# Optimization experiments

Hardware: AMD Instinct MI355X
Metric: run time of the kernel (lower is better)

Reference implementation:

```python
import jax, jax.numpy as jnp
import numpy as np

B, H, N, D = 2, 16, 2048, 64


def setup_inputs() -> dict:
    key = jax.random.key(0)
    kq, kk, kv = jax.random.split(key, 3)
    q = jax.random.normal(kq, (B, H, N, D), dtype=jnp.float32)
    k = jax.random.normal(kk, (B, H, N, D), dtype=jnp.float32)
    v = jax.random.normal(kv, (B, H, N, D), dtype=jnp.float32)
    return {"q": q, "k": k, "v": v}


def reference(q, k, v):
    b, h, n, d = q.shape
    # add_zero_kv: prepend an all-zero key/value along the sequence dim
    k = jnp.pad(k, ((0, 0), (0, 0), (1, 0), (0, 0)))  # [b,h,n+1,d]
    v = jnp.pad(v, ((0, 0), (0, 0), (1, 0), (0, 0)))
    kv_len = n + 1

    # l2_distance augmentation: q'.k' = 2 q.k - |q|^2 - |k|^2 = -|q - k|^2
    k_sq = jnp.sum(k * k, axis=-1, keepdims=True)
    k_aug = jnp.concatenate([k, -jnp.ones_like(k_sq), k_sq], axis=-1)  # [b,h,kv,d+2]
    q_sq = jnp.sum(q * q, axis=-1, keepdims=True)
    q_aug = jnp.concatenate([2.0 * q, q_sq, -jnp.ones_like(q_sq)], axis=-1)  # [b,h,n,d+2]

    # SDPA default scale uses the AUGMENTED head dim (d + 2)
    scale = (d + 2) ** -0.5
    scores = jnp.einsum('bhid,bhjd->bhij', q_aug, k_aug) * scale  # [b,h,n,kv]

    # causal mask folded into boolean mask because kv_len > q_len:
    # create_causal_mask(n, kv) = triu(ones, kv - n + 1) masked; allowed where j <= i + (kv - n)
    i = jnp.arange(n)[:, None]
    j = jnp.arange(kv_len)[None, :]
    allowed = j <= i + (kv_len - n)  # [n, kv]

    neg = jnp.asarray(-jnp.inf, dtype=scores.dtype)
    scores = jnp.where(allowed[None, None], scores, neg)
    attn = jax.nn.softmax(scores, axis=-1)
    out = jnp.einsum('bhij,bhjd->bhid', attn, v)  # [b,h,n,d]
    return out
```

## Files before the change

### kernel.cpp

```cpp
#include <hip/hip_runtime.h>


#define NQ 2048
#define DH 64
#define NT 32

typedef float f32x4 __attribute__((ext_vector_type(4)));
typedef __bf16 bf16x8 __attribute__((ext_vector_type(8)));
typedef unsigned short u16x8 __attribute__((ext_vector_type(8)));

union B8 { u16x8 u; bf16x8 b; };

__device__ __forceinline__ unsigned short f2b(float f) {
  unsigned int x = __builtin_bit_cast(unsigned int, f);
  unsigned int r = x + 0x7fffu + ((x >> 16) & 1u);
  return (unsigned short)(r >> 16);
}
__device__ __forceinline__ float b2f(unsigned short u) {
  unsigned int t = ((unsigned int)u) << 16;
  return __builtin_bit_cast(float, t);
}

__device__ __forceinline__ int kslot(int a) {
  return (a & 0x23) | ((a & 0x04) << 2) | ((a & 0x18) >> 1);
}

__device__ __forceinline__ void gl_lds16(const void* g, void* l) {
  __builtin_amdgcn_global_load_lds(
      (const __attribute__((address_space(1))) unsigned int*)g,
      (__attribute__((address_space(3))) unsigned int*)l, 16, 0, 0);
}
__device__ __forceinline__ void gl_lds4(const void* g, void* l) {
  __builtin_amdgcn_global_load_lds(
      (const __attribute__((address_space(1))) unsigned int*)g,
      (__attribute__((address_space(3))) unsigned int*)l, 4, 0, 0);
}

constexpr float QS = 0.3551784733906239f;
constexpr float BS = 0.17758923669531197f;

__global__ __launch_bounds__(256) void build_ws(
    const float* __restrict__ k, const float* __restrict__ v,
    unsigned short* __restrict__ wsK, unsigned short* __restrict__ wsV,
    float* __restrict__ wsB)
{
  const int bh = blockIdx.x;
  const int t  = blockIdx.y;
  const int tid  = threadIdx.x;
  const int wid  = tid >> 6;
  const int lane = tid & 63;
  const size_t bhN = (size_t)bh * NQ;
  const int tile64 = t * 64;
  const size_t tileId = (size_t)bh * NT + t;
  unsigned short* Kt = wsK + tileId * 4096;
  unsigned short* Vt = wsV + tileId * 4096;
  float*          Bt = wsB + tileId * 64;

  __shared__ float sTb[64];

#pragma unroll
  for (int i = 0; i < 4; i++) {
    int f  = i * 256 + tid;
    int kg = f >> 4, d4 = f & 15;
    int slot = kslot(kg);
    const float4* kp = (const float4*)(k + (bhN + tile64 + kg) * DH);
    float4 kk = kp[d4];
    unsigned short h0 = f2b(kk.x), h1 = f2b(kk.y), h2 = f2b(kk.z), h3 = f2b(kk.w);
    float a0 = b2f(h0), a1 = b2f(h1), a2 = b2f(h2), a3 = b2f(h3);
    float ss = a0*a0 + a1*a1 + a2*a2 + a3*a3;
    ss += __shfl_xor(ss, 1, 64);
    ss += __shfl_xor(ss, 2, 64);
    ss += __shfl_xor(ss, 4, 64);
    ss += __shfl_xor(ss, 8, 64);
    if (d4 == 0) {
      float tb = __builtin_amdgcn_exp2f(-BS * ss);
      Bt[slot] = tb;
      sTb[kg]  = tb;
    }
    unsigned int w0 = (unsigned int)h0 | ((unsigned int)h1 << 16);
    unsigned int w1 = (unsigned int)h2 | ((unsigned int)h3 << 16);
    int idx = slot * 64 + ((d4 * 4) ^ ((slot & 7) << 3));
    uint2 wv; wv.x = w0; wv.y = w1;
    *(uint2*)&Kt[idx] = wv;
  }
  __syncthreads();

#pragma unroll
  for (int jj = 0; jj < 4; jj++) {
    int kgb = jj * 16 + wid * 4;
    const float* vp = v + (bhN + tile64 + kgb) * DH + lane;
    float x0 = vp[0] * sTb[kgb + 0];
    float x1 = vp[DH] * sTb[kgb + 1];
    float x2 = vp[2 * DH] * sTb[kgb + 2];
    float x3 = vp[3 * DH] * sTb[kgb + 3];
    unsigned int w0 = (unsigned int)f2b(x0) | ((unsigned int)f2b(x1) << 16);
    unsigned int w1 = (unsigned int)f2b(x2) | ((unsigned int)f2b(x3) << 16);
    int idx = lane * 64 + (kgb ^ ((lane & 7) << 3));
    uint2 wv; wv.x = w0; wv.y = w1;
    *(uint2*)&Vt[idx] = wv;
  }
}

__global__ __launch_bounds__(256) void attend_l2_flash(
    const float* __restrict__ q,
    const unsigned short* __restrict__ wsK,
    const unsigned short* __restrict__ wsV,
    const float* __restrict__ wsB,
    float* __restrict__ out)
{
  const int bh   = blockIdx.x;
  const int qt   = (gridDim.y - 1) - blockIdx.y;
  const int qbase = qt * 64;
  const int tid  = threadIdx.x;
  const int wid  = tid >> 6;
  const int lane = tid & 63;
  const int g    = lane >> 4;
  const int qi   = lane & 15;
  const int qg   = qbase + wid * 16 + qi;
  const size_t bhN = (size_t)bh * NQ;

  __shared__ __align__(16) unsigned short sK[2][4096];
  __shared__ __align__(16) unsigned short sV[2][4096];
  __shared__ __align__(16) float sB[2][64];

  const float* qrow = q + (bhN + qg) * DH;
  bf16x8 q8[2];
#pragma unroll
  for (int ks = 0; ks < 2; ks++) {
    B8 th;
#pragma unroll
    for (int j = 0; j < 8; j++)
      th.u[j] = f2b(qrow[ks * 32 + g * 8 + j] * QS);
    q8[ks] = th.b;
  }

  f32x4 oacc[4] = { {0,0,0,0}, {0,0,0,0}, {0,0,0,0}, {0,0,0,0} };
  f32x4 l4 = {0, 0, 0, 0};

  const int ntiles = qt + 1;
  const size_t tbase = (size_t)bh * NT;

  auto STAGE = [&](int buf, int t) {
    const char* Kt = (const char*)(wsK + (tbase + t) * 4096);
    const char* Vt = (const char*)(wsV + (tbase + t) * 4096);
#pragma unroll
    for (int c = 0; c < 2; c++) {
      int boff = wid * 2048 + c * 1024;
      gl_lds16(Kt + boff + lane * 16, (char*)&sK[buf][0] + boff);
      gl_lds16(Vt + boff + lane * 16, (char*)&sV[buf][0] + boff);
    }
    if (wid == 0) {
      const char* Bt = (const char*)(wsB + (tbase + t) * 64);
      gl_lds4(Bt + lane * 4, (char*)&sB[buf][0]);
    }
  };

  int cur = 0;
  STAGE(0, 0);
  __syncthreads();

  for (int t = 0; t < ntiles; t++) {
    if (t + 1 < ntiles) STAGE(cur ^ 1, t + 1);

    f32x4 sc[4] = { {0,0,0,0}, {0,0,0,0}, {0,0,0,0}, {0,0,0,0} };
#pragma unroll
    for (int c = 0; c < 4; c++) {
#pragma unroll
      for (int ks = 0; ks < 2; ks++) {
        int idx = (16 * c + qi) * 64 + ((ks * 32 + g * 8) ^ ((qi & 7) << 3));
        bf16x8 ak = *(const bf16x8*)&sK[cur][idx];
        sc[c] = __builtin_amdgcn_mfma_f32_16x16x32_bf16(ak, q8[ks], sc[c], 0, 0, 0);
      }
    }

    const bool diag = (t == ntiles - 1);
    if (diag) {
      const int tile64 = t * 64;
#pragma unroll
      for (int c = 0; c < 4; c++)
#pragma unroll
        for (int r = 0; r < 4; r++) {
          int key = tile64 + 32 * (c >> 1) + 8 * g + 4 * (c & 1) + r;
          if (key > qg) sc[c][r] = -1e30f;
        }
    }

#pragma unroll
    for (int c = 0; c < 4; c++) {
      f32x4 tb = *(const f32x4*)&sB[cur][16 * c + 4 * g];
#pragma unroll
      for (int r = 0; r < 4; r++) sc[c][r] = __builtin_amdgcn_exp2f(sc[c][r]);
#pragma unroll
      for (int r = 0; r < 4; r++) l4[r] = __builtin_fmaf(sc[c][r], tb[r], l4[r]);
    }

    B8 t0, t1;
#pragma unroll
    for (int j = 0; j < 8; j++) {
      t0.b[j] = (__bf16)sc[(j >> 2)][j & 3];
      t1.b[j] = (__bf16)sc[2 + (j >> 2)][j & 3];
    }

#pragma unroll
    for (int db = 0; db < 4; db++) {
#pragma unroll
      for (int ks = 0; ks < 2; ks++) {
        int idx = (db * 16 + qi) * 64 + ((ks * 32 + g * 8) ^ ((qi & 7) << 3));
        bf16x8 av = *(const bf16x8*)&sV[cur][idx];
        oacc[db] = __builtin_amdgcn_mfma_f32_16x16x32_bf16(av, (ks ? t1.b : t0.b),
                                                           oacc[db], 0, 0, 0);
      }
    }
    __syncthreads();
    cur ^= 1;
  }

  float lt = (l4[0] + l4[1]) + (l4[2] + l4[3]);
  lt += __shfl_xor(lt, 16, 64);
  lt += __shfl_xor(lt, 32, 64);
  float denom = lt + 1.0f;
  float inv = 1.0f / denom;
  float* op = out + (bhN + qg) * DH;
#pragma unroll
  for (int db = 0; db < 4; db++) {
    float4 o;
    o.x = oacc[db][0] * inv;
    o.y = oacc[db][1] * inv;
    o.z = oacc[db][2] * inv;
    o.w = oacc[db][3] * inv;
    *(float4*)(op + db * 16 + 4 * g) = o;
  }
}

extern "C" void kernel_launch(void* const* d_in, const int* in_sizes, int n_in,
                              void* d_out, int out_size, void* d_ws, size_t ws_size,
                              hipStream_t stream) {
  (void)in_sizes; (void)n_in; (void)out_size; (void)ws_size;
  const float* q = (const float*)d_in[0];
  const float* k = (const float*)d_in[1];
  const float* v = (const float*)d_in[2];
  float* out = (float*)d_out;

  char* ws = (char*)d_ws;
  unsigned short* wsK = (unsigned short*)ws;
  unsigned short* wsV = (unsigned short*)(ws + (8u << 20));
  float*          wsB = (float*)(ws + (16u << 20));

  build_ws<<<dim3(32, NT), dim3(256), 0, stream>>>(k, v, wsK, wsV, wsB);
  attend_l2_flash<<<dim3(32, NT), dim3(256), 0, stream>>>(q, wsK, wsV, wsB, out);
}
```

Baseline: 52.61 us.

## Triple-buffer K/V tiles with manual vmcnt waits and register-load bias terms

New measurement: 49.15 us, median of 2. 1.07x faster.

```diff
diff --git a/kernel.cpp b/kernel.cpp
--- a/kernel.cpp
+++ b/kernel.cpp
@@ -29,11 +29,6 @@
   __builtin_amdgcn_global_load_lds(
       (const __attribute__((address_space(1))) unsigned int*)g,
       (__attribute__((address_space(3))) unsigned int*)l, 16, 0, 0);
-}
-__device__ __forceinline__ void gl_lds4(const void* g, void* l) {
-  __builtin_amdgcn_global_load_lds(
-      (const __attribute__((address_space(1))) unsigned int*)g,
-      (__attribute__((address_space(3))) unsigned int*)l, 4, 0, 0);
 }
 
 constexpr float QS = 0.3551784733906239f;
@@ -119,9 +114,8 @@
   const int qg   = qbase + wid * 16 + qi;
   const size_t bhN = (size_t)bh * NQ;
 
-  __shared__ __align__(16) unsigned short sK[2][4096];
-  __shared__ __align__(16) unsigned short sV[2][4096];
-  __shared__ __align__(16) float sB[2][64];
+  __shared__ __align__(16) unsigned short sK[3][4096];
+  __shared__ __align__(16) unsigned short sV[3][4096];
 
   const float* qrow = q + (bhN + qg) * DH;
   bf16x8 q8[2];
@@ -139,28 +133,45 @@
 
   const int ntiles = qt + 1;
   const size_t tbase = (size_t)bh * NT;
-
-  auto STAGE = [&](int buf, int t) {
+  const float* TB = wsB + tbase * 64;
+
+  auto LTB = [&](int t, f32x4* tb) {
+    const float* p = TB + t * 64 + 4 * g;
+#pragma unroll
+    for (int c = 0; c < 4; c++) tb[c] = *(const f32x4*)(p + 16 * c);
+  };
+  auto STAGE = [&](unsigned short* bK, unsigned short* bV, int t) {
     const char* Kt = (const char*)(wsK + (tbase + t) * 4096);
     const char* Vt = (const char*)(wsV + (tbase + t) * 4096);
 #pragma unroll
     for (int c = 0; c < 2; c++) {
       int boff = wid * 2048 + c * 1024;
-      gl_lds16(Kt + boff + lane * 16, (char*)&sK[buf][0] + boff);
-      gl_lds16(Vt + boff + lane * 16, (char*)&sV[buf][0] + boff);
-    }
-    if (wid == 0) {
-      const char* Bt = (const char*)(wsB + (tbase + t) * 64);
-      gl_lds4(Bt + lane * 4, (char*)&sB[buf][0]);
+      gl_lds16(Kt + boff + lane * 16, (char*)bK + boff);
+      gl_lds16(Vt + boff + lane * 16, (char*)bV + boff);
     }
   };
 
-  int cur = 0;
-  STAGE(0, 0);
-  __syncthreads();
+  unsigned short *kA = sK[0], *kB = sK[1], *kC = sK[2];
+  unsigned short *vA = sV[0], *vB = sV[1], *vC = sV[2];
+  f32x4 tb_cur[4], tb_nxt[4];
+
+  STAGE(kA, vA, 0);
+  LTB(0, tb_cur);
+  if (ntiles > 1) {
+    STAGE(kB, vB, 1);
+    asm volatile("s_waitcnt vmcnt(4)" ::: "memory");
+  } else {
+    asm volatile("s_waitcnt vmcnt(0)" ::: "memory");
+  }
+  __builtin_amdgcn_s_barrier();
 
   for (int t = 0; t < ntiles; t++) {
-    if (t + 1 < ntiles) STAGE(cur ^ 1, t + 1);
+    const bool hasN1 = (t + 1 < ntiles);
+    const bool hasN2 = (t + 2 < ntiles);
+    if (hasN1) LTB(t + 1, tb_nxt);
+    __builtin_amdgcn_sched_barrier(0);
+    if (hasN2) STAGE(kC, vC, t + 2);
+    __builtin_amdgcn_sched_barrier(0);
 
     f32x4 sc[4] = { {0,0,0,0}, {0,0,0,0}, {0,0,0,0}, {0,0,0,0} };
 #pragma unroll
@@ -168,13 +179,12 @@
 #pragma unroll
       for (int ks = 0; ks < 2; ks++) {
         int idx = (16 * c + qi) * 64 + ((ks * 32 + g * 8) ^ ((qi & 7) << 3));
-        bf16x8 ak = *(const bf16x8*)&sK[cur][idx];
+        bf16x8 ak = *(const bf16x8*)&kA[idx];
         sc[c] = __builtin_amdgcn_mfma_f32_16x16x32_bf16(ak, q8[ks], sc[c], 0, 0, 0);
       }
     }
 
-    const bool diag = (t == ntiles - 1);
-    if (diag) {
+    if (t == ntiles - 1) {
       const int tile64 = t * 64;
 #pragma unroll
       for (int c = 0; c < 4; c++)
@@ -187,11 +197,10 @@
 
 #pragma unroll
     for (int c = 0; c < 4; c++) {
-      f32x4 tb = *(const f32x4*)&sB[cur][16 * c + 4 * g];
 #pragma unroll
       for (int r = 0; r < 4; r++) sc[c][r] = __builtin_amdgcn_exp2f(sc[c][r]);
 #pragma unroll
-      for (int r = 0; r < 4; r++) l4[r] = __builtin_fmaf(sc[c][r], tb[r], l4[r]);
+      for (int r = 0; r < 4; r++) l4[r] = __builtin_fmaf(sc[c][r], tb_cur[c][r], l4[r]);
     }
 
     B8 t0, t1;
@@ -206,13 +215,20 @@
 #pragma unroll
       for (int ks = 0; ks < 2; ks++) {
         int idx = (db * 16 + qi) * 64 + ((ks * 32 + g * 8) ^ ((qi & 7) << 3));
-        bf16x8 av = *(const bf16x8*)&sV[cur][idx];
+        bf16x8 av = *(const bf16x8*)&vA[idx];
         oacc[db] = __builtin_amdgcn_mfma_f32_16x16x32_bf16(av, (ks ? t1.b : t0.b),
                                                            oacc[db], 0, 0, 0);
       }
     }
-    __syncthreads();
-    cur ^= 1;
+
+    if (hasN2) asm volatile("s_waitcnt vmcnt(4)" ::: "memory");
+    else       asm volatile("s_waitcnt vmcnt(0)" ::: "memory");
+    __builtin_amdgcn_s_barrier();
+
+    unsigned short* tk = kA; kA = kB; kB = kC; kC = tk;
+    unsigned short* tv = vA; vA = vB; vB = vC; vC = tv;
+#pragma unroll
+    for (int c = 0; c < 4; c++) tb_cur[c] = tb_nxt[c];
   }
 
   float lt = (l4[0] + l4[1]) + (l4[2] + l4[3]);
```
